# Kernel tuning notes

Measured on AMD Instinct MI355X. Metric: run time of the kernel, lower is better.

Reference implementation:

```python
import jax, jax.numpy as jnp
import numpy as np

H_LAT = 64   # latent height (original_shape H)
W_LAT = 64   # latent width  (original_shape W)
COND_LEN = 77  # text tokens per regional condition


def _resize_nearest_exact(m, H, W):
    # matches torch F.interpolate(mode='nearest-exact') for a 2D mask
    h0, w0 = m.shape
    ih = jnp.floor((jnp.arange(H) + 0.5) * (h0 / H)).astype(jnp.int32)
    iw = jnp.floor((jnp.arange(W) + 0.5) * (w0 / W)).astype(jnp.int32)
    return m[ih][:, iw]


def setup_inputs() -> dict:
    key = jax.random.key(0)
    kq, kk, kv, km = jax.random.split(key, 4)
    b, qlen, inner = 2, H_LAT * W_LAT, 512
    klen = 4 * COND_LEN  # 4 regions x 77 tokens
    q = jax.random.normal(kq, (b, qlen, inner), dtype=jnp.float32)
    k = jax.random.normal(kk, (b, klen, inner), dtype=jnp.float32)
    v = jax.random.normal(kv, (b, klen, inner), dtype=jnp.float32)
    dd_masks = jax.random.uniform(km, (4, 32, 32), dtype=jnp.float32)
    # ensure full spatial coverage (region 0 = global) so no softmax row is all-masked
    dd_masks = dd_masks.at[0].set(1.0)
    return {"q": q, "k": k, "v": v, "dd_masks": dd_masks, "heads": 8}


def reference(q, k, v, dd_masks, heads):
    b, qlen, inner = q.shape
    dh = inner // heads
    # [b, heads, seq, dh]
    qh = q.reshape(b, qlen, heads, dh).transpose(0, 2, 1, 3)
    kh = k.reshape(b, -1, heads, dh).transpose(0, 2, 1, 3)
    vh = v.reshape(b, -1, heads, dh).transpose(0, 2, 1, 3)

    # build DenseDiffusion mask: each region mask resized to HxW, flattened,
    # and repeated over that region's COND_LEN key columns
    R = dd_masks.shape[0]
    resized = jax.vmap(lambda m: _resize_nearest_exact(m, H_LAT, W_LAT))(dd_masks)  # [R,H,W]
    flat = resized.reshape(R, H_LAT * W_LAT).T            # [HW, R]
    masks = jnp.repeat(flat, COND_LEN, axis=1)            # [HW, R*COND_LEN]
    mask_bool = masks > 0.5                               # [HW, klen]
    mask_scale = (H_LAT * W_LAT) / jnp.sum(masks, axis=0, keepdims=True)  # [1, klen]

    scale = 1.0 / np.sqrt(dh).astype(np.float32)
    attn = jnp.einsum('bhqd,bhkd->bhqk', qh, kh) * scale  # [b,h,HW,klen]
    attn = attn * mask_scale                              # broadcast over b,h,q
    attn = jnp.where(mask_bool, attn, -jnp.inf)
    w = jax.nn.softmax(attn, axis=-1)
    out = jnp.einsum('bhqk,bhkd->bhqd', w, vh)
    return out.transpose(0, 2, 1, 3).reshape(b, qlen, heads * dh)
```

## Files before the change

kernel.cpp:

```cpp
#include <hip/hip_runtime.h>
#include <hip/hip_bf16.h>

typedef __attribute__((ext_vector_type(8))) short short8;
typedef __attribute__((ext_vector_type(4))) float floatx4;

#define HW_TOK 4096
#define KLEN 308
#define DH 64
#define INNER 512

#define KROWS 320
#define VSTRU 328
#define VBASE (KROWS * 64)
#define KV_TOTAL (VBASE + DH * VSTRU)
#define PSTR 40

__device__ __forceinline__ unsigned short f2bf(float f) {
    union { float f; unsigned u; } x; x.f = f;
    unsigned u = x.u;
    return (unsigned short)((u + 0x7FFFu + ((u >> 16) & 1u)) >> 16);
}
__device__ __forceinline__ unsigned pk2bf(float a, float b) {
    return ((unsigned)f2bf(b) << 16) | (unsigned)f2bf(a);
}

__global__ __launch_bounds__(512, 1)
void dd_attn_kernel(const float* __restrict__ q,
                    const float* __restrict__ k,
                    const float* __restrict__ v,
                    const float* __restrict__ dd,
                    float* __restrict__ out) {
    __shared__ unsigned short KV[KV_TOTAL];
    __shared__ unsigned short Pb[8][2][16][PSTR];

    const int tid  = threadIdx.x;
    const int lane = tid & 63;
    const int wave = tid >> 6;
    const int quad = lane >> 4;
    const int l15  = lane & 15;

    const int bid = blockIdx.x;
    const int bh  = bid >> 4;
    const int grp = bid & 15;
    const int b = bh >> 3, h = bh & 7;

    const float* qp = q + (size_t)b * HW_TOK * INNER + h * DH;
    const float* kp = k + (size_t)b * KLEN * INNER + h * DH;
    const float* vp = v + (size_t)b * KLEN * INNER + h * DH;
    float* op = out + (size_t)b * HW_TOK * INNER + h * DH;

    for (int e = tid; e < KLEN * 32; e += 512) {
        int row = e >> 5, d2 = e & 31;
        float2 f = *(const float2*)(kp + (size_t)row * INNER + 2 * d2);
        int c = d2 >> 2;
        int off = row * 64 + (((c ^ (row & 7)) << 3) | ((d2 & 3) << 1));
        *(unsigned*)&KV[off] = pk2bf(f.x, f.y);
    }
    #pragma unroll
    for (int i = 0; i < 5; ++i) {
        int cq = wave + 8 * i;
        float f[8];
        #pragma unroll
        for (int j = 0; j < 8; ++j) {
            int col = cq * 8 + j;
            f[j] = (col < KLEN) ? vp[(size_t)col * INNER + lane] : 0.f;
        }
        union { short8 s; unsigned u[4]; } vv;
        #pragma unroll
        for (int j = 0; j < 4; ++j) vv.u[j] = pk2bf(f[2 * j], f[2 * j + 1]);
        int swz = (cq & ~7) | ((cq ^ (lane & 7)) & 7);
        *(short8*)&KV[VBASE + lane * VSTRU + (swz << 3)] = vv.s;
    }
    float rsum = 0.f;
    {
        const float* dp = dd + quad * 1024 + l15 * 4;
        #pragma unroll
        for (int j = 0; j < 16; ++j) {
            float4 f = *(const float4*)(dp + j * 64);
            rsum += f.x + f.y + f.z + f.w;
        }
        #pragma unroll
        for (int off = 1; off < 16; off <<= 1) rsum += __shfl_xor(rsum, off);
    }
    float rsc[4];
    #pragma unroll
    for (int r = 0; r < 4; ++r)
        rsc[r] = 4096.0f / (4.0f * __shfl(rsum, r * 16 + l15));

    __syncthreads();

    const int q0 = (grp * 8 + wave) * 32;

    short8 qa[2][2];
    #pragma unroll
    for (int qt = 0; qt < 2; ++qt) {
        const float* qr = qp + (size_t)(q0 + qt * 16 + l15) * INNER + quad * 8;
        float4 g0 = *(const float4*)(qr);
        float4 g1 = *(const float4*)(qr + 4);
        float4 g2 = *(const float4*)(qr + 32);
        float4 g3 = *(const float4*)(qr + 36);
        union { short8 s; unsigned u[4]; } ua, ub;
        ua.u[0] = pk2bf(g0.x, g0.y); ua.u[1] = pk2bf(g0.z, g0.w);
        ua.u[2] = pk2bf(g1.x, g1.y); ua.u[3] = pk2bf(g1.z, g1.w);
        ub.u[0] = pk2bf(g2.x, g2.y); ub.u[1] = pk2bf(g2.z, g2.w);
        ub.u[2] = pk2bf(g3.x, g3.y); ub.u[3] = pk2bf(g3.z, g3.w);
        qa[qt][0] = ua.s; qa[qt][1] = ub.s;
    }
    float coef[2][4];
    #pragma unroll
    for (int qt = 0; qt < 2; ++qt) {
        int qrow = q0 + qt * 16 + l15;
        int mi = (qrow >> 7) * 32 + ((qrow & 63) >> 1);
        #pragma unroll
        for (int r = 0; r < 4; ++r)
            coef[qt][r] = (dd[r * 1024 + mi] > 0.5f) ? 0.125f * rsc[r] : -1.0f;
    }

    float m_run[2] = {-INFINITY, -INFINITY};
    float l_run[2] = {0.f, 0.f};
    floatx4 oacc[2][4] = {{{0,0,0,0},{0,0,0,0},{0,0,0,0},{0,0,0,0}},
                          {{0,0,0,0},{0,0,0,0},{0,0,0,0},{0,0,0,0}}};

    #pragma unroll
    for (int ch = 0; ch < 4; ++ch) {
        const int NT = (ch < 3) ? 6 : 2;
        floatx4 acc[2][6];

        #pragma unroll
        for (int t = 0; t < NT; ++t) {
            int row = (ch * 6 + t) * 16 + l15;
            short8 ka0 = *(const short8*)&KV[row * 64 + (((quad    ) ^ (row & 7)) << 3)];
            short8 ka1 = *(const short8*)&KV[row * 64 + (((4 + quad) ^ (row & 7)) << 3)];
            #pragma unroll
            for (int qt = 0; qt < 2; ++qt) {
                floatx4 c = {0.f, 0.f, 0.f, 0.f};
                c = __builtin_amdgcn_mfma_f32_16x16x32_bf16(ka0, qa[qt][0], c, 0, 0, 0);
                c = __builtin_amdgcn_mfma_f32_16x16x32_bf16(ka1, qa[qt][1], c, 0, 0, 0);
                acc[qt][t] = c;
            }
        }

        #pragma unroll
        for (int qt = 0; qt < 2; ++qt) {
            float mloc = -INFINITY;
            #pragma unroll
            for (int t = 0; t < NT; ++t) {
                #pragma unroll
                for (int r = 0; r < 4; ++r) {
                    int kc = (ch * 6 + t) * 16 + quad * 4 + r;
                    float cf = (kc < 77) ? coef[qt][0] : (kc < 154) ? coef[qt][1]
                             : (kc < 231) ? coef[qt][2] : (kc < 308) ? coef[qt][3] : -1.0f;
                    float sv = (cf > 0.f) ? acc[qt][t][r] * cf : -INFINITY;
                    acc[qt][t][r] = sv;
                    mloc = fmaxf(mloc, sv);
                }
            }
            mloc = fmaxf(mloc, __shfl_xor(mloc, 16));
            mloc = fmaxf(mloc, __shfl_xor(mloc, 32));
            float m_new = fmaxf(m_run[qt], mloc);
            float alpha = __expf(m_run[qt] - m_new);
            float lloc = 0.f;
            #pragma unroll
            for (int t = 0; t < NT; ++t) {
                #pragma unroll
                for (int r = 0; r < 4; ++r) {
                    float p = __expf(acc[qt][t][r] - m_new);
                    acc[qt][t][r] = p;
                    lloc += p;
                }
            }
            lloc += __shfl_xor(lloc, 16);
            lloc += __shfl_xor(lloc, 32);
            l_run[qt] = l_run[qt] * alpha + lloc;
            m_run[qt] = m_new;
            #pragma unroll
            for (int n = 0; n < 4; ++n)
                #pragma unroll
                for (int r = 0; r < 4; ++r) oacc[qt][n][r] *= alpha;
        }

        const int NS = NT / 2;
        #pragma unroll
        for (int s = 0; s < NS; ++s) {
            #pragma unroll
            for (int qt = 0; qt < 2; ++qt) {
                unsigned p0 = pk2bf(acc[qt][2*s][0],     acc[qt][2*s][1]);
                unsigned p1 = pk2bf(acc[qt][2*s][2],     acc[qt][2*s][3]);
                unsigned p2 = pk2bf(acc[qt][2*s+1][0],   acc[qt][2*s+1][1]);
                unsigned p3 = pk2bf(acc[qt][2*s+1][2],   acc[qt][2*s+1][3]);
                *(uint2*)&Pb[wave][qt][l15][quad * 4]      = make_uint2(p0, p1);
                *(uint2*)&Pb[wave][qt][l15][16 + quad * 4] = make_uint2(p2, p3);
            }
            short8 pbv[2];
            #pragma unroll
            for (int qt = 0; qt < 2; ++qt)
                pbv[qt] = *(const short8*)&Pb[wave][qt][l15][quad * 8];
            #pragma unroll
            for (int n = 0; n < 4; ++n) {
                int row = n * 16 + l15;
                int cq = ch * 12 + s * 4 + quad;
                int swz = (cq & ~7) | ((cq ^ (row & 7)) & 7);
                short8 va = *(const short8*)&KV[VBASE + row * VSTRU + (swz << 3)];
                #pragma unroll
                for (int qt = 0; qt < 2; ++qt)
                    oacc[qt][n] = __builtin_amdgcn_mfma_f32_16x16x32_bf16(va, pbv[qt], oacc[qt][n], 0, 0, 0);
            }
        }
    }

    #pragma unroll
    for (int qt = 0; qt < 2; ++qt) {
        float inv = 1.0f / l_run[qt];
        float* o = op + (size_t)(q0 + qt * 16 + l15) * INNER + quad * 4;
        #pragma unroll
        for (int n = 0; n < 4; ++n) {
            float4 ov;
            ov.x = oacc[qt][n][0] * inv;
            ov.y = oacc[qt][n][1] * inv;
            ov.z = oacc[qt][n][2] * inv;
            ov.w = oacc[qt][n][3] * inv;
            *(float4*)&o[n * 16] = ov;
        }
    }
}

extern "C" void kernel_launch(void* const* d_in, const int* in_sizes, int n_in,
                              void* d_out, int out_size, void* d_ws, size_t ws_size,
                              hipStream_t stream) {
    const float* q  = (const float*)d_in[0];
    const float* k  = (const float*)d_in[1];
    const float* v  = (const float*)d_in[2];
    const float* dd = (const float*)d_in[3];
    float* out = (float*)d_out;
    dd_attn_kernel<<<dim3(256), dim3(512), 0, stream>>>(q, k, v, dd, out);
}
```

Baseline: 93.59 us.

## Double waves per block, each wave handling one 16-row query tile

Raises the block to 1024 threads (16 waves), with each wave processing a single 16-query tile instead of two. The K/V staging load is split across twice as many threads, and the padding K rows (308..319) are now zeroed in shared memory. The aim is more waves in flight to hide memory and MFMA latency, and a shorter per-block staging phase. In exchange, each K/V fragment read from LDS feeds only one MFMA instead of two, so LDS traffic per unit of compute roughly doubles.

```diff
diff --git a/kernel.cpp b/kernel.cpp
--- a/kernel.cpp
+++ b/kernel.cpp
@@ -14,6 +14,7 @@
 #define VBASE (KROWS * 64)
 #define KV_TOTAL (VBASE + DH * VSTRU)
 #define PSTR 40
+#define NWAVES 16
 
 __device__ __forceinline__ unsigned short f2bf(float f) {
     union { float f; unsigned u; } x; x.f = f;
@@ -24,14 +25,14 @@
     return ((unsigned)f2bf(b) << 16) | (unsigned)f2bf(a);
 }
 
-__global__ __launch_bounds__(512, 1)
+__global__ __launch_bounds__(1024, 1)
 void dd_attn_kernel(const float* __restrict__ q,
                     const float* __restrict__ k,
                     const float* __restrict__ v,
                     const float* __restrict__ dd,
                     float* __restrict__ out) {
     __shared__ unsigned short KV[KV_TOTAL];
-    __shared__ unsigned short Pb[8][2][16][PSTR];
+    __shared__ unsigned short Pb[NWAVES][16][PSTR];
 
     const int tid  = threadIdx.x;
     const int lane = tid & 63;
@@ -49,27 +50,31 @@
     const float* vp = v + (size_t)b * KLEN * INNER + h * DH;
     float* op = out + (size_t)b * HW_TOK * INNER + h * DH;
 
-    for (int e = tid; e < KLEN * 32; e += 512) {
+    for (int e = tid; e < KLEN * 32; e += 1024) {
         int row = e >> 5, d2 = e & 31;
         float2 f = *(const float2*)(kp + (size_t)row * INNER + 2 * d2);
         int c = d2 >> 2;
         int off = row * 64 + (((c ^ (row & 7)) << 3) | ((d2 & 3) << 1));
         *(unsigned*)&KV[off] = pk2bf(f.x, f.y);
     }
-    #pragma unroll
-    for (int i = 0; i < 5; ++i) {
-        int cq = wave + 8 * i;
-        float f[8];
-        #pragma unroll
-        for (int j = 0; j < 8; ++j) {
-            int col = cq * 8 + j;
-            f[j] = (col < KLEN) ? vp[(size_t)col * INNER + lane] : 0.f;
-        }
-        union { short8 s; unsigned u[4]; } vv;
-        #pragma unroll
-        for (int j = 0; j < 4; ++j) vv.u[j] = pk2bf(f[2 * j], f[2 * j + 1]);
-        int swz = (cq & ~7) | ((cq ^ (lane & 7)) & 7);
-        *(short8*)&KV[VBASE + lane * VSTRU + (swz << 3)] = vv.s;
+    for (int e = tid; e < 12 * 64; e += 1024) KV[KLEN * 64 + e] = 0;
+
+    #pragma unroll
+    for (int i = 0; i < 3; ++i) {
+        int cq = wave + NWAVES * i;
+        if (cq < 40) {
+            float f[8];
+            #pragma unroll
+            for (int j = 0; j < 8; ++j) {
+                int col = cq * 8 + j;
+                f[j] = (col < KLEN) ? vp[(size_t)col * INNER + lane] : 0.f;
+            }
+            union { short8 s; unsigned u[4]; } vv;
+            #pragma unroll
+            for (int j = 0; j < 4; ++j) vv.u[j] = pk2bf(f[2 * j], f[2 * j + 1]);
+            int swz = (cq & ~7) | ((cq ^ (lane & 7)) & 7);
+            *(short8*)&KV[VBASE + lane * VSTRU + (swz << 3)] = vv.s;
+        }
     }
     float rsum = 0.f;
     {
@@ -89,138 +94,116 @@
 
     __syncthreads();
 
-    const int q0 = (grp * 8 + wave) * 32;
-
-    short8 qa[2][2];
-    #pragma unroll
-    for (int qt = 0; qt < 2; ++qt) {
-        const float* qr = qp + (size_t)(q0 + qt * 16 + l15) * INNER + quad * 8;
-        float4 g0 = *(const float4*)(qr);
-        float4 g1 = *(const float4*)(qr + 4);
-        float4 g2 = *(const float4*)(qr + 32);
-        float4 g3 = *(const float4*)(qr + 36);
+    const int q0 = (grp * NWAVES + wave) * 16;
+    const int qrow = q0 + l15;
+
+    const float* qr = qp + (size_t)qrow * INNER + quad * 8;
+    float4 g0 = *(const float4*)(qr);
+    float4 g1 = *(const float4*)(qr + 4);
+    float4 g2 = *(const float4*)(qr + 32);
+    float4 g3 = *(const float4*)(qr + 36);
+    short8 qa0, qa1;
+    {
         union { short8 s; unsigned u[4]; } ua, ub;
         ua.u[0] = pk2bf(g0.x, g0.y); ua.u[1] = pk2bf(g0.z, g0.w);
         ua.u[2] = pk2bf(g1.x, g1.y); ua.u[3] = pk2bf(g1.z, g1.w);
         ub.u[0] = pk2bf(g2.x, g2.y); ub.u[1] = pk2bf(g2.z, g2.w);
         ub.u[2] = pk2bf(g3.x, g3.y); ub.u[3] = pk2bf(g3.z, g3.w);
-        qa[qt][0] = ua.s; qa[qt][1] = ub.s;
-    }
-    float coef[2][4];
-    #pragma unroll
-    for (int qt = 0; qt < 2; ++qt) {
-        int qrow = q0 + qt * 16 + l15;
-        int mi = (qrow >> 7) * 32 + ((qrow & 63) >> 1);
-        #pragma unroll
-        for (int r = 0; r < 4; ++r)
-            coef[qt][r] = (dd[r * 1024 + mi] > 0.5f) ? 0.125f * rsc[r] : -1.0f;
-    }
-
-    float m_run[2] = {-INFINITY, -INFINITY};
-    float l_run[2] = {0.f, 0.f};
-    floatx4 oacc[2][4] = {{{0,0,0,0},{0,0,0,0},{0,0,0,0},{0,0,0,0}},
-                          {{0,0,0,0},{0,0,0,0},{0,0,0,0},{0,0,0,0}}};
+        qa0 = ua.s; qa1 = ub.s;
+    }
+
+    const int mi = (qrow >> 7) * 32 + ((qrow & 63) >> 1);
+    float coef[4];
+    #pragma unroll
+    for (int r = 0; r < 4; ++r)
+        coef[r] = (dd[r * 1024 + mi] > 0.5f) ? 0.125f * rsc[r] : -1.0f;
+
+    float m_run = -INFINITY, l_run = 0.f;
+    floatx4 oacc[4] = {{0,0,0,0},{0,0,0,0},{0,0,0,0},{0,0,0,0}};
 
     #pragma unroll
     for (int ch = 0; ch < 4; ++ch) {
         const int NT = (ch < 3) ? 6 : 2;
-        floatx4 acc[2][6];
+        floatx4 acc[6];
 
         #pragma unroll
         for (int t = 0; t < NT; ++t) {
             int row = (ch * 6 + t) * 16 + l15;
             short8 ka0 = *(const short8*)&KV[row * 64 + (((quad    ) ^ (row & 7)) << 3)];
             short8 ka1 = *(const short8*)&KV[row * 64 + (((4 + quad) ^ (row & 7)) << 3)];
-            #pragma unroll
-            for (int qt = 0; qt < 2; ++qt) {
-                floatx4 c = {0.f, 0.f, 0.f, 0.f};
-                c = __builtin_amdgcn_mfma_f32_16x16x32_bf16(ka0, qa[qt][0], c, 0, 0, 0);
-                c = __builtin_amdgcn_mfma_f32_16x16x32_bf16(ka1, qa[qt][1], c, 0, 0, 0);
-                acc[qt][t] = c;
-            }
-        }
-
-        #pragma unroll
-        for (int qt = 0; qt < 2; ++qt) {
-            float mloc = -INFINITY;
-            #pragma unroll
-            for (int t = 0; t < NT; ++t) {
-                #pragma unroll
-                for (int r = 0; r < 4; ++r) {
-                    int kc = (ch * 6 + t) * 16 + quad * 4 + r;
-                    float cf = (kc < 77) ? coef[qt][0] : (kc < 154) ? coef[qt][1]
-                             : (kc < 231) ? coef[qt][2] : (kc < 308) ? coef[qt][3] : -1.0f;
-                    float sv = (cf > 0.f) ? acc[qt][t][r] * cf : -INFINITY;
-                    acc[qt][t][r] = sv;
-                    mloc = fmaxf(mloc, sv);
-                }
-            }
-            mloc = fmaxf(mloc, __shfl_xor(mloc, 16));
-            mloc = fmaxf(mloc, __shfl_xor(mloc, 32));
-            float m_new = fmaxf(m_run[qt], mloc);
-            float alpha = __expf(m_run[qt] - m_new);
-            float lloc = 0.f;
-            #pragma unroll
-            for (int t = 0; t < NT; ++t) {
-                #pragma unroll
-                for (int r = 0; r < 4; ++r) {
-                    float p = __expf(acc[qt][t][r] - m_new);
-                    acc[qt][t][r] = p;
-                    lloc += p;
-                }
-            }
-            lloc += __shfl_xor(lloc, 16);
-            lloc += __shfl_xor(lloc, 32);
-            l_run[qt] = l_run[qt] * alpha + lloc;
-            m_run[qt] = m_new;
-            #pragma unroll
-            for (int n = 0; n < 4; ++n)
-                #pragma unroll
-                for (int r = 0; r < 4; ++r) oacc[qt][n][r] *= alpha;
-        }
+            floatx4 c = {0.f, 0.f, 0.f, 0.f};
+            c = __builtin_amdgcn_mfma_f32_16x16x32_bf16(ka0, qa0, c, 0, 0, 0);
+            c = __builtin_amdgcn_mfma_f32_16x16x32_bf16(ka1, qa1, c, 0, 0, 0);
+            acc[t] = c;
+        }
+
+        float mloc = -INFINITY;
+        #pragma unroll
+        for (int t = 0; t < NT; ++t) {
+            #pragma unroll
+            for (int r = 0; r < 4; ++r) {
+                int kc = (ch * 6 + t) * 16 + quad * 4 + r;
+                float cf = (kc < 77) ? coef[0] : (kc < 154) ? coef[1]
+                         : (kc < 231) ? coef[2] : (kc < 308) ? coef[3] : -1.0f;
+                float sv = (cf > 0.f) ? acc[t][r] * cf : -INFINITY;
+                acc[t][r] = sv;
+                mloc = fmaxf(mloc, sv);
+            }
+        }
+        mloc = fmaxf(mloc, __shfl_xor(mloc, 16));
+        mloc = fmaxf(mloc, __shfl_xor(mloc, 32));
+        float m_new = fmaxf(m_run, mloc);
+        float alpha = __expf(m_run - m_new);
+        float lloc = 0.f;
+        #pragma unroll
+        for (int t = 0; t < NT; ++t) {
+            #pragma unroll
+            for (int r = 0; r < 4; ++r) {
+                float p = __expf(acc[t][r] - m_new);
+                acc[t][r] = p;
+                lloc += p;
+            }
+        }
+        lloc += __shfl_xor(lloc, 16);
+        lloc += __shfl_xor(lloc, 32);
+        l_run = l_run * alpha + lloc;
+        m_run = m_new;
+        #pragma unroll
+        for (int n = 0; n < 4; ++n)
+            #pragma unroll
+            for (int r = 0; r < 4; ++r) oacc[n][r] *= alpha;
 
         const int NS = NT / 2;
         #pragma unroll
         for (int s = 0; s < NS; ++s) {
-            #pragma unroll
-            for (int qt = 0; qt < 2; ++qt) {
-                unsigned p0 = pk2bf(acc[qt][2*s][0],     acc[qt][2*s][1]);
-                unsigned p1 = pk2bf(acc[qt][2*s][2],     acc[qt][2*s][3]);
-                unsigned p2 = pk2bf(acc[qt][2*s+1][0],   acc[qt][2*s+1][1]);
-                unsigned p3 = pk2bf(acc[qt][2*s+1][2],   acc[qt][2*s+1][3]);
-                *(uint2*)&Pb[wave][qt][l15][quad * 4]      = make_uint2(p0, p1);
-                *(uint2*)&Pb[wave][qt][l15][16 + quad * 4] = make_uint2(p2, p3);
-            }
-            short8 pbv[2];
-            #pragma unroll
-            for (int qt = 0; qt < 2; ++qt)
-                pbv[qt] = *(const short8*)&Pb[wave][qt][l15][quad * 8];
+            unsigned p0 = pk2bf(acc[2*s][0],   acc[2*s][1]);
+            unsigned p1 = pk2bf(acc[2*s][2],   acc[2*s][3]);
+            unsigned p2 = pk2bf(acc[2*s+1][0], acc[2*s+1][1]);
+            unsigned p3 = pk2bf(acc[2*s+1][2], acc[2*s+1][3]);
+            *(uint2*)&Pb[wave][l15][quad * 4]      = make_uint2(p0, p1);
+            *(uint2*)&Pb[wave][l15][16 + quad * 4] = make_uint2(p2, p3);
+            short8 pbv = *(const short8*)&Pb[wave][l15][quad * 8];
             #pragma unroll
             for (int n = 0; n < 4; ++n) {
                 int row = n * 16 + l15;
                 int cq = ch * 12 + s * 4 + quad;
                 int swz = (cq & ~7) | ((cq ^ (row & 7)) & 7);
                 short8 va = *(const short8*)&KV[VBASE + row * VSTRU + (swz << 3)];
-                #pragma unroll
-                for (int qt = 0; qt < 2; ++qt)
-                    oacc[qt][n] = __builtin_amdgcn_mfma_f32_16x16x32_bf16(va, pbv[qt], oacc[qt][n], 0, 0, 0);
-            }
-        }
-    }
-
-    #pragma unroll
-    for (int qt = 0; qt < 2; ++qt) {
-        float inv = 1.0f / l_run[qt];
-        float* o = op + (size_t)(q0 + qt * 16 + l15) * INNER + quad * 4;
-        #pragma unroll
-        for (int n = 0; n < 4; ++n) {
-            float4 ov;
-            ov.x = oacc[qt][n][0] * inv;
-            ov.y = oacc[qt][n][1] * inv;
-            ov.z = oacc[qt][n][2] * inv;
-            ov.w = oacc[qt][n][3] * inv;
-            *(float4*)&o[n * 16] = ov;
-        }
+                oacc[n] = __builtin_amdgcn_mfma_f32_16x16x32_bf16(va, pbv, oacc[n], 0, 0, 0);
+            }
+        }
+    }
+
+    const float inv = 1.0f / l_run;
+    float* o = op + (size_t)qrow * INNER + quad * 4;
+    #pragma unroll
+    for (int n = 0; n < 4; ++n) {
+        float4 ov;
+        ov.x = oacc[n][0] * inv;
+        ov.y = oacc[n][1] * inv;
+        ov.z = oacc[n][2] * inv;
+        ov.w = oacc[n][3] * inv;
+        *(float4*)&o[n * 16] = ov;
     }
 }
 
@@ -232,5 +215,5 @@
     const float* v  = (const float*)d_in[2];
     const float* dd = (const float*)d_in[3];
     float* out = (float*)d_out;
-    dd_attn_kernel<<<dim3(256), dim3(512), 0, stream>>>(q, k, v, dd, out);
-}
+    dd_attn_kernel<<<dim3(256), dim3(1024), 0, stream>>>(q, k, v, dd, out);
+}
```

Measured after the change: 93.19 us. Within noise of the previous version (-0.4%).
